# Optimization experiments

Hardware: AMD Instinct MI355X
Metric: run time of the kernel (lower is better)

Reference implementation:

```python
import jax, jax.numpy as jnp
import numpy as np

GLYPH_DIM = 4096
PADDING_IDX = GLYPH_DIM  # 4096
GLYPH_EMB = 20           # CHAR_EMB 16 + COLOR_EMB 4
HIDDEN = 32
MAX_LEN = 64


def setup_inputs() -> dict:
    key = jax.random.key(0)
    k1, k2, k3, k4, k5, k6, k7 = jax.random.split(key, 7)
    B, H, W = 8192, 21, 79
    glyph_chars = jax.random.randint(k1, (B, H, W), 0, 256, dtype=jnp.int32)
    glyph_colors = jax.random.randint(k2, (B, H, W), 0, 16, dtype=jnp.int32)
    # Embedding table with zero padding row (torch padding_idx semantics)
    emb_table = jax.random.normal(k3, (GLYPH_DIM + 1, GLYPH_EMB), dtype=jnp.float32) * 0.02
    emb_table = emb_table.at[PADDING_IDX].set(0.0)
    s = 1.0 / np.sqrt(HIDDEN)
    W_ih = jax.random.uniform(k4, (HIDDEN, GLYPH_EMB), minval=-s, maxval=s, dtype=jnp.float32)
    W_hh = jax.random.uniform(k5, (HIDDEN, HIDDEN), minval=-s, maxval=s, dtype=jnp.float32)
    b_ih = jax.random.uniform(k6, (HIDDEN,), minval=-s, maxval=s, dtype=jnp.float32)
    b_hh = jax.random.uniform(k7, (HIDDEN,), minval=-s, maxval=s, dtype=jnp.float32)
    return {"glyph_chars": glyph_chars, "glyph_colors": glyph_colors,
            "emb_table": emb_table, "W_ih": W_ih, "W_hh": W_hh,
            "b_ih": b_ih, "b_hh": b_hh}


def _encode_bag(glyph_chars, glyph_colors):
    """Batched sorted-unique compaction over the bounded glyph id range."""
    B = glyph_chars.shape[0]
    g_ids = ((glyph_chars << 4) + glyph_colors).reshape(B, -1)  # [B, H*W]
    # presence[b, g] = glyph g appears in sample b (batched histogram)
    bidx = jnp.broadcast_to(jnp.arange(B, dtype=g_ids.dtype)[:, None], g_ids.shape)
    presence = jnp.zeros((B, GLYPH_DIM), dtype=bool).at[bidx, g_ids].set(True)
    # compact: present ids keep their value, absent become PADDING_IDX (=4096),
    # so sorting yields ascending unique ids followed by padding.
    ids = jnp.arange(GLYPH_DIM, dtype=jnp.int32)
    keys = jnp.where(presence, ids, jnp.int32(PADDING_IDX))
    bag = jnp.sort(keys, axis=1)[:, :MAX_LEN]  # [B, MAX_LEN]
    lengths = jnp.minimum(presence.sum(axis=1), MAX_LEN)  # [B]
    return bag, lengths


def reference(glyph_chars, glyph_colors, emb_table, W_ih, W_hh, b_ih, b_hh):
    bag, lengths = _encode_bag(glyph_chars, glyph_colors)
    emb = emb_table[bag]  # [B, MAX_LEN, GLYPH_EMB]
    B = emb.shape[0]

    # packed RNN == plain RNN where hidden state freezes past each sequence length
    xs = jnp.swapaxes(emb, 0, 1)  # [T, B, E]

    def step(h, inp):
        xt, t = inp
        h_new = jnp.tanh(xt @ W_ih.T + b_ih + h @ W_hh.T + b_hh)
        h = jnp.where((t < lengths)[:, None], h_new, h)
        return h, None

    h0 = jnp.zeros((B, HIDDEN), dtype=emb.dtype)
    h, _ = jax.lax.scan(step, h0, (xs, jnp.arange(MAX_LEN)))
    return (h, emb, bag)
```

## Files before the change

### kernel.cpp

```cpp
#include <hip/hip_runtime.h>

#define HW 1659
#define PADID 4096
#define EMB 20
#define HID 32
#define MAXLEN 64

typedef float v2f __attribute__((ext_vector_type(2)));

template <int CTRL>
__device__ __forceinline__ float dppf(float v) {
    return __builtin_bit_cast(float,
        __builtin_amdgcn_update_dpp(0, __builtin_bit_cast(int, v),
                                    CTRL, 0xF, 0xF, true));
}
#define DPP_XOR1 0xB1
#define DPP_XOR2 0x4E
#define DPP_XOR7 0x141
#define DPP_XORF 0x140

__global__ __launch_bounds__(128) void proj_kernel(
    const float* __restrict__ emb_table, const float* __restrict__ W_ih,
    float* __restrict__ proj)
{
    const int tid = threadIdx.x;
    const int g = blockIdx.x * 4 + (tid >> 5);
    const int j = tid & 31;
    if (g > PADID) return;
    const float* er = emb_table + (size_t)g * EMB;
    const float* wr = W_ih + j * EMB;
    float s = 0.f;
#pragma unroll
    for (int k = 0; k < EMB; k++) s += wr[k] * er[k];
    proj[(size_t)g * HID + j] = s;
}

__global__ __launch_bounds__(256) void bag_emb_kernel(
    const int* __restrict__ chars, const int* __restrict__ colors,
    const float* __restrict__ emb_table,
    float* __restrict__ out_emb, float* __restrict__ out_bag)
{
    __shared__ unsigned char pres[4096];
    __shared__ int bagl[64];
    __shared__ int wsum[4];

    const int b   = blockIdx.x;
    const int tid = threadIdx.x;
    const int lane = tid & 63;
    const int wv   = tid >> 6;

    const int base = b * HW;
    const int pe = (4 - (base & 3)) & 3;
    const int nv = (HW - pe) >> 2;
    const int nt = HW - pe - (nv << 2);
    const int4* c4 = (const int4*)(chars + base + pe);
    const int4* k4 = (const int4*)(colors + base + pe);

    int4 ca = c4[tid], ka = k4[tid];
    const bool has2 = (tid + 256) < nv;
    const int i2 = has2 ? tid + 256 : tid;
    int4 cb = c4[i2], kb = k4[i2];
    int gp = -1, gt = -1;
    if (tid < pe) gp = (chars[base + tid] << 4) + colors[base + tid];
    if (tid < nt) {
        int i = base + pe + (nv << 2) + tid;
        gt = (chars[i] << 4) + colors[i];
    }

    ((uint4*)pres)[tid] = make_uint4(0u, 0u, 0u, 0u);
    if (tid < 64) bagl[tid] = PADID;
    __syncthreads();

    pres[(ca.x << 4) + ka.x] = 1;
    pres[(ca.y << 4) + ka.y] = 1;
    pres[(ca.z << 4) + ka.z] = 1;
    pres[(ca.w << 4) + ka.w] = 1;
    if (has2) {
        pres[(cb.x << 4) + kb.x] = 1;
        pres[(cb.y << 4) + kb.y] = 1;
        pres[(cb.z << 4) + kb.z] = 1;
        pres[(cb.w << 4) + kb.w] = 1;
    }
    if (gp >= 0) pres[gp] = 1;
    if (gt >= 0) pres[gt] = 1;
    __syncthreads();

    uint4 w4 = ((const uint4*)pres)[tid];
    const unsigned M = 0x01010101u;
    int cnt = __popc(w4.x & M) + __popc(w4.y & M)
            + __popc(w4.z & M) + __popc(w4.w & M);

    int pre = cnt;
#pragma unroll
    for (int d = 1; d < 64; d <<= 1) {
        int v = __shfl_up(pre, d, 64);
        if (lane >= d) pre += v;
    }
    if (lane == 63) wsum[wv] = pre;
    __syncthreads();
    int wbase = 0;
#pragma unroll
    for (int w2 = 0; w2 < 4; w2++) wbase += (w2 < wv) ? wsum[w2] : 0;
    int p = wbase + pre - cnt;

    unsigned wrd[4] = {w4.x, w4.y, w4.z, w4.w};
#pragma unroll
    for (int c = 0; c < 4; c++) {
#pragma unroll
        for (int k = 0; k < 4; k++) {
            if ((wrd[c] >> (8 * k)) & 1) {
                if (p < 64) bagl[p] = 16 * tid + 4 * c + k;
                p++;
            }
        }
    }
    __syncthreads();

    if (tid < 64) out_bag[(size_t)b * 64 + tid] = (float)bagl[tid];

    const float4* tab4 = (const float4*)emb_table;
    float4* dst4 = (float4*)(out_emb + (size_t)b * (MAXLEN * EMB));
    for (int q = tid; q < MAXLEN * 5; q += 256) {
        int t = q / 5;
        int m = q - t * 5;
        int row = bagl[t];
        dst4[q] = tab4[row * 5 + m];
    }
}

__global__ __launch_bounds__(128)
__attribute__((amdgpu_waves_per_eu(2, 2)))
void rnn_kernel(
    const float* __restrict__ proj, const float* __restrict__ bagf,
    const float* __restrict__ W_hh,
    const float* __restrict__ b_ih, const float* __restrict__ b_hh,
    float* __restrict__ out_h)
{
    const int tid  = threadIdx.x;
    const int wv   = tid >> 6;
    const int lane = tid & 63;
    const int sl   = lane >> 4;
    const int ib   = wv * 4 + sl;
    const int jj   = lane & 15;
    const int b    = blockIdx.x * 8 + ib;

    const int GMAP[16] = {0,1,2,3, 7,6,5,4, 15,14,13,12,11,10,9,8};

    v2f w0[16], w1[16];
    const float2* wr0 = (const float2*)(W_hh + (2 * jj) * HID);
    const float2* wr1 = (const float2*)(W_hh + (2 * jj + 1) * HID);
#pragma unroll
    for (int m = 0; m < 16; m++) {
        const int c = jj ^ GMAP[m];
        float2 a = wr0[c], bb = wr1[c];
        w0[m] = (v2f){a.x, a.y};
        w1[m] = (v2f){bb.x, bb.y};
    }
    const float sb0 = b_ih[2 * jj]     + b_hh[2 * jj];
    const float sb1 = b_ih[2 * jj + 1] + b_hh[2 * jj + 1];

    const float* bps = bagf + (size_t)b * 64;
    const float2* proj2 = (const float2*)proj;

    float h0 = 0.f, h1 = 0.f;

#pragma unroll
    for (int ch = 0; ch < 4; ch++) {
        int idx[16];
#pragma unroll
        for (int i = 0; i < 16; i++) idx[i] = (int)bps[ch * 16 + i];
        float2 pv[16];
#pragma unroll
        for (int i = 0; i < 16; i++) pv[i] = proj2[idx[i] * 16 + jj];

#pragma unroll
        for (int i = 0; i < 16; i++) {
            const bool upd = idx[i] < PADID;

            v2f g[16];
            g[0] = (v2f){h0, h1};
            g[1] = (v2f){dppf<DPP_XOR1>(g[0].x), dppf<DPP_XOR1>(g[0].y)};
            g[2] = (v2f){dppf<DPP_XOR2>(g[0].x), dppf<DPP_XOR2>(g[0].y)};
            g[3] = (v2f){dppf<DPP_XOR2>(g[1].x), dppf<DPP_XOR2>(g[1].y)};
#pragma unroll
            for (int m = 0; m < 4; m++)
                g[4 + m] = (v2f){dppf<DPP_XOR7>(g[m].x), dppf<DPP_XOR7>(g[m].y)};
#pragma unroll
            for (int m = 0; m < 8; m++)
                g[8 + m] = (v2f){dppf<DPP_XORF>(g[m].x), dppf<DPP_XORF>(g[m].y)};

            v2f a0 = (v2f){0.f, 0.f}, b0 = a0, a1 = a0, b1 = a0;
#pragma unroll
            for (int m = 0; m < 16; m += 2) {
                a0 = __builtin_elementwise_fma(w0[m],     g[m],     a0);
                b0 = __builtin_elementwise_fma(w0[m + 1], g[m + 1], b0);
                a1 = __builtin_elementwise_fma(w1[m],     g[m],     a1);
                b1 = __builtin_elementwise_fma(w1[m + 1], g[m + 1], b1);
            }
            float s0 = sb0 + pv[i].x + (a0.x + a0.y) + (b0.x + b0.y);
            float s1 = sb1 + pv[i].y + (a1.x + a1.y) + (b1.x + b1.y);

            float e0 = __expf(2.f * s0);
            float e1 = __expf(2.f * s1);
            float th0 = 1.f - 2.f * __builtin_amdgcn_rcpf(e0 + 1.f);
            float th1 = 1.f - 2.f * __builtin_amdgcn_rcpf(e1 + 1.f);

            h0 = upd ? th0 : h0;
            h1 = upd ? th1 : h1;
        }
    }

    ((float2*)(out_h + (size_t)b * HID))[jj] = make_float2(h0, h1);
}

__global__ __launch_bounds__(128, 4) void rnn_kernel_noproj(
    const float* __restrict__ emb, const float* __restrict__ bagf,
    const float* __restrict__ W_ih, const float* __restrict__ W_hh,
    const float* __restrict__ b_ih, const float* __restrict__ b_hh,
    float* __restrict__ out_h)
{
    __shared__ float hbuf[4][32];
    const int tid = threadIdx.x;
    const int ib  = tid >> 5;
    const int j   = tid & 31;
    const int b   = blockIdx.x * 4 + ib;

    float wih[EMB];
#pragma unroll
    for (int k = 0; k < EMB; k++) wih[k] = W_ih[j * EMB + k];
    float whh[HID];
#pragma unroll
    for (int k = 0; k < HID; k++) whh[k] = W_hh[j * HID + k];
    const float sbias = b_ih[j] + b_hh[j];

    const float* bp = bagf + (size_t)b * 64;
    unsigned long long m0 = __ballot(bp[j]      < 4095.5f);
    unsigned long long m1 = __ballot(bp[32 + j] < 4095.5f);
    const int half = ib & 1;
    const int len = __popc((unsigned)(m0 >> (half * 32)))
                  + __popc((unsigned)(m1 >> (half * 32)));

    hbuf[ib][j] = 0.f;
    asm volatile("s_waitcnt lgkmcnt(0)" ::: "memory");

    float h = 0.f;
    const float* xb = emb + (size_t)b * (MAXLEN * EMB);
    for (int t = 0; t < MAXLEN; t++) {
        const float4* xp = (const float4*)(xb + t * EMB);
        float4 x0 = xp[0], x1 = xp[1], x2 = xp[2], x3 = xp[3], x4 = xp[4];
        float s = sbias;
        const float4* hb4 = (const float4*)hbuf[ib];
#pragma unroll
        for (int m = 0; m < 8; m++) {
            float4 hv = hb4[m];
            s += whh[4*m+0]*hv.x + whh[4*m+1]*hv.y
               + whh[4*m+2]*hv.z + whh[4*m+3]*hv.w;
        }
        s += wih[0]*x0.x + wih[1]*x0.y + wih[2]*x0.z + wih[3]*x0.w;
        s += wih[4]*x1.x + wih[5]*x1.y + wih[6]*x1.z + wih[7]*x1.w;
        s += wih[8]*x2.x + wih[9]*x2.y + wih[10]*x2.z + wih[11]*x2.w;
        s += wih[12]*x3.x + wih[13]*x3.y + wih[14]*x3.z + wih[15]*x3.w;
        s += wih[16]*x4.x + wih[17]*x4.y + wih[18]*x4.z + wih[19]*x4.w;
        s = fminf(fmaxf(s, -9.f), 9.f);
        float e = __expf(2.f * s);
        float th = (e - 1.f) * __builtin_amdgcn_rcpf(e + 1.f);
        h = (t < len) ? th : h;
        hbuf[ib][j] = h;
        asm volatile("s_waitcnt lgkmcnt(0)" ::: "memory");
    }
    out_h[(size_t)b * HID + j] = h;
}

extern "C" void kernel_launch(void* const* d_in, const int* in_sizes, int n_in,
                              void* d_out, int out_size, void* d_ws, size_t ws_size,
                              hipStream_t stream) {
    const int*   chars     = (const int*)d_in[0];
    const int*   colors    = (const int*)d_in[1];
    const float* emb_table = (const float*)d_in[2];
    const float* W_ih      = (const float*)d_in[3];
    const float* W_hh      = (const float*)d_in[4];
    const float* b_ih      = (const float*)d_in[5];
    const float* b_hh      = (const float*)d_in[6];

    const int B = in_sizes[0] / HW;

    float* out     = (float*)d_out;
    float* out_h   = out;
    float* out_emb = out + (size_t)B * HID;
    float* out_bag = out_emb + (size_t)B * MAXLEN * EMB;

    const size_t proj_bytes = (size_t)(PADID + 1) * HID * sizeof(float);

    bag_emb_kernel<<<B, 256, 0, stream>>>(chars, colors, emb_table, out_emb, out_bag);

    if (ws_size >= proj_bytes) {
        float* proj = (float*)d_ws;
        proj_kernel<<<(PADID + 1 + 3) / 4, 128, 0, stream>>>(emb_table, W_ih, proj);
        rnn_kernel<<<B / 8, 128, 0, stream>>>(proj, out_bag, W_hh, b_ih, b_hh, out_h);
    } else {
        rnn_kernel_noproj<<<B / 4, 128, 0, stream>>>(out_emb, out_bag, W_ih, W_hh,
                                                     b_ih, b_hh, out_h);
    }
}
```

Measured before the change: 179.8 us.

## Assign one wave per bag sample and fuse projection into bag kernel

Restructures the bag/embedding kernel so each 64-lane wave handles one sample with its own 4KB presence table, which drops the block-wide __syncthreads and the cross-wave scan. The compaction now scans the presence table in four chunks and stops early once 64 ids are found. The separate proj_kernel launch is folded in as extra tail blocks of the same grid, saving one launch. In exchange each block uses 16KB of LDS, which can limit occupancy, and each wave issues more sequential loads per sample.

```diff
diff --git a/kernel.cpp b/kernel.cpp
--- a/kernel.cpp
+++ b/kernel.cpp
@@ -5,6 +5,7 @@
 #define EMB 20
 #define HID 32
 #define MAXLEN 64
+#define PROJ_BLOCKS 64
 
 typedef float v2f __attribute__((ext_vector_type(2)));
 
@@ -19,35 +20,40 @@
 #define DPP_XOR7 0x141
 #define DPP_XORF 0x140
 
-__global__ __launch_bounds__(128) void proj_kernel(
+__global__ __launch_bounds__(256, 8) void bag_emb_wave_kernel(
+    const int* __restrict__ chars, const int* __restrict__ colors,
     const float* __restrict__ emb_table, const float* __restrict__ W_ih,
-    float* __restrict__ proj)
+    float* __restrict__ out_emb, float* __restrict__ out_bag,
+    float* __restrict__ proj, int nbag, int Btot)
 {
-    const int tid = threadIdx.x;
-    const int g = blockIdx.x * 4 + (tid >> 5);
-    const int j = tid & 31;
-    if (g > PADID) return;
-    const float* er = emb_table + (size_t)g * EMB;
-    const float* wr = W_ih + j * EMB;
-    float s = 0.f;
-#pragma unroll
-    for (int k = 0; k < EMB; k++) s += wr[k] * er[k];
-    proj[(size_t)g * HID + j] = s;
-}
-
-__global__ __launch_bounds__(256) void bag_emb_kernel(
-    const int* __restrict__ chars, const int* __restrict__ colors,
-    const float* __restrict__ emb_table,
-    float* __restrict__ out_emb, float* __restrict__ out_bag)
-{
-    __shared__ unsigned char pres[4096];
-    __shared__ int bagl[64];
-    __shared__ int wsum[4];
-
-    const int b   = blockIdx.x;
-    const int tid = threadIdx.x;
+    if ((int)blockIdx.x >= nbag) {
+        const int gid = ((int)blockIdx.x - nbag) * 256 + threadIdx.x;
+        const int NP = (PADID + 1) * HID;
+        for (int idx = gid; idx < NP; idx += PROJ_BLOCKS * 256) {
+            const int g = idx >> 5, j = idx & 31;
+            const float* er = emb_table + (size_t)g * EMB;
+            const float* wr = W_ih + j * EMB;
+            float s = 0.f;
+#pragma unroll
+            for (int k = 0; k < EMB; k++) s += wr[k] * er[k];
+            proj[idx] = s;
+        }
+        return;
+    }
+
+    __shared__ __align__(16) unsigned char pres[4][4096];
+    __shared__ int bagl[4][64];
+
+    const int tid  = threadIdx.x;
+    const int wv   = tid >> 6;
     const int lane = tid & 63;
-    const int wv   = tid >> 6;
+    const int b    = (int)blockIdx.x * 4 + wv;
+    if (b >= Btot) return;
+
+    uint4* pz = (uint4*)pres[wv];
+#pragma unroll
+    for (int r = 0; r < 4; r++) pz[lane + (r << 6)] = make_uint4(0u, 0u, 0u, 0u);
+    bagl[wv][lane] = PADID;
 
     const int base = b * HW;
     const int pe = (4 - (base & 3)) & 3;
@@ -56,75 +62,75 @@
     const int4* c4 = (const int4*)(chars + base + pe);
     const int4* k4 = (const int4*)(colors + base + pe);
 
-    int4 ca = c4[tid], ka = k4[tid];
-    const bool has2 = (tid + 256) < nv;
-    const int i2 = has2 ? tid + 256 : tid;
-    int4 cb = c4[i2], kb = k4[i2];
     int gp = -1, gt = -1;
-    if (tid < pe) gp = (chars[base + tid] << 4) + colors[base + tid];
-    if (tid < nt) {
-        int i = base + pe + (nv << 2) + tid;
+    if (lane < pe) gp = (chars[base + lane] << 4) + colors[base + lane];
+    if (lane < nt) {
+        const int i = base + pe + (nv << 2) + lane;
         gt = (chars[i] << 4) + colors[i];
     }
 
-    ((uint4*)pres)[tid] = make_uint4(0u, 0u, 0u, 0u);
-    if (tid < 64) bagl[tid] = PADID;
-    __syncthreads();
-
-    pres[(ca.x << 4) + ka.x] = 1;
-    pres[(ca.y << 4) + ka.y] = 1;
-    pres[(ca.z << 4) + ka.z] = 1;
-    pres[(ca.w << 4) + ka.w] = 1;
-    if (has2) {
-        pres[(cb.x << 4) + kb.x] = 1;
-        pres[(cb.y << 4) + kb.y] = 1;
-        pres[(cb.z << 4) + kb.z] = 1;
-        pres[(cb.w << 4) + kb.w] = 1;
-    }
-    if (gp >= 0) pres[gp] = 1;
-    if (gt >= 0) pres[gt] = 1;
-    __syncthreads();
-
-    uint4 w4 = ((const uint4*)pres)[tid];
+    unsigned char* pw = pres[wv];
+#pragma unroll
+    for (int k = 0; k < 7; k++) {
+        const int i = lane + (k << 6);
+        if (i < nv) {
+            const int4 c = c4[i], kk = k4[i];
+            pw[(c.x << 4) + kk.x] = 1;
+            pw[(c.y << 4) + kk.y] = 1;
+            pw[(c.z << 4) + kk.z] = 1;
+            pw[(c.w << 4) + kk.w] = 1;
+        }
+    }
+    if (gp >= 0) pw[gp] = 1;
+    if (gt >= 0) pw[gt] = 1;
+
+    asm volatile("s_waitcnt lgkmcnt(0)" ::: "memory");
+
     const unsigned M = 0x01010101u;
-    int cnt = __popc(w4.x & M) + __popc(w4.y & M)
-            + __popc(w4.z & M) + __popc(w4.w & M);
-
-    int pre = cnt;
-#pragma unroll
-    for (int d = 1; d < 64; d <<= 1) {
-        int v = __shfl_up(pre, d, 64);
-        if (lane >= d) pre += v;
-    }
-    if (lane == 63) wsum[wv] = pre;
-    __syncthreads();
-    int wbase = 0;
-#pragma unroll
-    for (int w2 = 0; w2 < 4; w2++) wbase += (w2 < wv) ? wsum[w2] : 0;
-    int p = wbase + pre - cnt;
-
-    unsigned wrd[4] = {w4.x, w4.y, w4.z, w4.w};
-#pragma unroll
-    for (int c = 0; c < 4; c++) {
-#pragma unroll
-        for (int k = 0; k < 4; k++) {
-            if ((wrd[c] >> (8 * k)) & 1) {
-                if (p < 64) bagl[p] = 16 * tid + 4 * c + k;
-                p++;
+    int base_cnt = 0;
+#pragma unroll 1
+    for (int r = 0; r < 4; r++) {
+        const uint4 w = ((const uint4*)pres[wv])[lane + (r << 6)];
+        const int cnt = __popc(w.x & M) + __popc(w.y & M)
+                      + __popc(w.z & M) + __popc(w.w & M);
+        int pre = cnt;
+#pragma unroll
+        for (int d = 1; d < 64; d <<= 1) {
+            const int v = __shfl_up(pre, d, 64);
+            if (lane >= d) pre += v;
+        }
+        int p = base_cnt + pre - cnt;
+        if (p < 64 && cnt) {
+            const unsigned wd[4] = {w.x, w.y, w.z, w.w};
+            const int idbase = (r << 10) + (lane << 4);
+#pragma unroll
+            for (int c = 0; c < 4; c++) {
+                unsigned m = wd[c] & M;
+                while (m) {
+                    const int bit = __ffs((int)m) - 1;
+                    if (p < 64) bagl[wv][p] = idbase + (c << 2) + (bit >> 3);
+                    p++;
+                    m &= m - 1;
+                }
             }
         }
-    }
-    __syncthreads();
-
-    if (tid < 64) out_bag[(size_t)b * 64 + tid] = (float)bagl[tid];
+        base_cnt += __shfl(pre, 63, 64);
+        if (base_cnt >= 64) break;
+    }
+
+    asm volatile("s_waitcnt lgkmcnt(0)" ::: "memory");
+
+    out_bag[(size_t)b * 64 + lane] = (float)bagl[wv][lane];
 
     const float4* tab4 = (const float4*)emb_table;
     float4* dst4 = (float4*)(out_emb + (size_t)b * (MAXLEN * EMB));
-    for (int q = tid; q < MAXLEN * 5; q += 256) {
-        int t = q / 5;
-        int m = q - t * 5;
-        int row = bagl[t];
-        dst4[q] = tab4[row * 5 + m];
+#pragma unroll
+    for (int m5 = 0; m5 < 5; m5++) {
+        const int q = lane + (m5 << 6);
+        const int t = q / 5;
+        const int mm = q - t * 5;
+        const int row = bagl[wv][t];
+        dst4[q] = tab4[row * 5 + mm];
     }
 }
 
@@ -283,6 +289,7 @@
     const float* b_hh      = (const float*)d_in[6];
 
     const int B = in_sizes[0] / HW;
+    const int NBAG = (B + 3) / 4;
 
     float* out     = (float*)d_out;
     float* out_h   = out;
@@ -291,13 +298,14 @@
 
     const size_t proj_bytes = (size_t)(PADID + 1) * HID * sizeof(float);
 
-    bag_emb_kernel<<<B, 256, 0, stream>>>(chars, colors, emb_table, out_emb, out_bag);
-
-    if (ws_size >= proj_bytes) {
+    if (ws_size >= proj_bytes && (B % 8) == 0) {
         float* proj = (float*)d_ws;
-        proj_kernel<<<(PADID + 1 + 3) / 4, 128, 0, stream>>>(emb_table, W_ih, proj);
+        bag_emb_wave_kernel<<<NBAG + PROJ_BLOCKS, 256, 0, stream>>>(
+            chars, colors, emb_table, W_ih, out_emb, out_bag, proj, NBAG, B);
         rnn_kernel<<<B / 8, 128, 0, stream>>>(proj, out_bag, W_hh, b_ih, b_hh, out_h);
     } else {
+        bag_emb_wave_kernel<<<NBAG, 256, 0, stream>>>(
+            chars, colors, emb_table, W_ih, out_emb, out_bag, (float*)d_ws, NBAG, B);
         rnn_kernel_noproj<<<B / 4, 128, 0, stream>>>(out_emb, out_bag, W_ih, W_hh,
                                                      b_ih, b_hh, out_h);
     }
```

Result: slower. 204.3 us (+13.7%).

## Fuse projection into bag kernel, halve block size, early-exit scan

Applied to the files above, without the earlier changes.

Merges the proj_kernel launch into bag_emb_kernel by appending extra blocks that compute the embedding-times-W_ih table, which removes one kernel launch. The bag kernel drops from 256 to 128 threads per block, so each thread loads four int4 vectors instead of two. The presence scan now walks the 4096-entry bitmap in two halves and stops once 64 unique ids have been found. The aim is lower launch overhead and less scan work, at the cost of more per-thread work and an extra barrier per half of the scan.

```diff
diff --git a/kernel.cpp b/kernel.cpp
--- a/kernel.cpp
+++ b/kernel.cpp
@@ -5,6 +5,7 @@
 #define EMB 20
 #define HID 32
 #define MAXLEN 64
+#define PROJ_BLOCKS 128
 
 typedef float v2f __attribute__((ext_vector_type(2)));
 
@@ -19,35 +20,36 @@
 #define DPP_XOR7 0x141
 #define DPP_XORF 0x140
 
-__global__ __launch_bounds__(128) void proj_kernel(
+__global__ __launch_bounds__(128, 4) void bag_emb_kernel(
+    const int* __restrict__ chars, const int* __restrict__ colors,
     const float* __restrict__ emb_table, const float* __restrict__ W_ih,
-    float* __restrict__ proj)
+    float* __restrict__ out_emb, float* __restrict__ out_bag,
+    float* __restrict__ proj, int nbag)
 {
     const int tid = threadIdx.x;
-    const int g = blockIdx.x * 4 + (tid >> 5);
-    const int j = tid & 31;
-    if (g > PADID) return;
-    const float* er = emb_table + (size_t)g * EMB;
-    const float* wr = W_ih + j * EMB;
-    float s = 0.f;
-#pragma unroll
-    for (int k = 0; k < EMB; k++) s += wr[k] * er[k];
-    proj[(size_t)g * HID + j] = s;
-}
-
-__global__ __launch_bounds__(256) void bag_emb_kernel(
-    const int* __restrict__ chars, const int* __restrict__ colors,
-    const float* __restrict__ emb_table,
-    float* __restrict__ out_emb, float* __restrict__ out_bag)
-{
-    __shared__ unsigned char pres[4096];
+
+    if ((int)blockIdx.x >= nbag) {
+        const int gid = ((int)blockIdx.x - nbag) * 128 + tid;
+        const int NP = (PADID + 1) * HID;
+        for (int idx = gid; idx < NP; idx += PROJ_BLOCKS * 128) {
+            const int g = idx >> 5, j = idx & 31;
+            const float* er = emb_table + (size_t)g * EMB;
+            const float* wr = W_ih + j * EMB;
+            float s = 0.f;
+#pragma unroll
+            for (int k = 0; k < EMB; k++) s += wr[k] * er[k];
+            proj[idx] = s;
+        }
+        return;
+    }
+
+    __shared__ __align__(16) unsigned char pres[4096];
     __shared__ int bagl[64];
-    __shared__ int wsum[4];
-
-    const int b   = blockIdx.x;
-    const int tid = threadIdx.x;
+    __shared__ int wsum[2];
+
     const int lane = tid & 63;
     const int wv   = tid >> 6;
+    const int b    = blockIdx.x;
 
     const int base = b * HW;
     const int pe = (4 - (base & 3)) & 3;
@@ -56,63 +58,80 @@
     const int4* c4 = (const int4*)(chars + base + pe);
     const int4* k4 = (const int4*)(colors + base + pe);
 
-    int4 ca = c4[tid], ka = k4[tid];
-    const bool has2 = (tid + 256) < nv;
-    const int i2 = has2 ? tid + 256 : tid;
-    int4 cb = c4[i2], kb = k4[i2];
+    int4 ca0 = c4[tid],       ka0 = k4[tid];
+    int4 ca1 = c4[tid + 128], ka1 = k4[tid + 128];
+    int4 ca2 = c4[tid + 256], ka2 = k4[tid + 256];
+    const bool has3 = (tid + 384) < nv;
+    const int i3 = has3 ? tid + 384 : tid;
+    int4 ca3 = c4[i3], ka3 = k4[i3];
     int gp = -1, gt = -1;
     if (tid < pe) gp = (chars[base + tid] << 4) + colors[base + tid];
     if (tid < nt) {
-        int i = base + pe + (nv << 2) + tid;
+        const int i = base + pe + (nv << 2) + tid;
         gt = (chars[i] << 4) + colors[i];
     }
 
-    ((uint4*)pres)[tid] = make_uint4(0u, 0u, 0u, 0u);
+    ((uint4*)pres)[tid]       = make_uint4(0u, 0u, 0u, 0u);
+    ((uint4*)pres)[tid + 128] = make_uint4(0u, 0u, 0u, 0u);
     if (tid < 64) bagl[tid] = PADID;
     __syncthreads();
 
-    pres[(ca.x << 4) + ka.x] = 1;
-    pres[(ca.y << 4) + ka.y] = 1;
-    pres[(ca.z << 4) + ka.z] = 1;
-    pres[(ca.w << 4) + ka.w] = 1;
-    if (has2) {
-        pres[(cb.x << 4) + kb.x] = 1;
-        pres[(cb.y << 4) + kb.y] = 1;
-        pres[(cb.z << 4) + kb.z] = 1;
-        pres[(cb.w << 4) + kb.w] = 1;
+    pres[(ca0.x << 4) + ka0.x] = 1;
+    pres[(ca0.y << 4) + ka0.y] = 1;
+    pres[(ca0.z << 4) + ka0.z] = 1;
+    pres[(ca0.w << 4) + ka0.w] = 1;
+    pres[(ca1.x << 4) + ka1.x] = 1;
+    pres[(ca1.y << 4) + ka1.y] = 1;
+    pres[(ca1.z << 4) + ka1.z] = 1;
+    pres[(ca1.w << 4) + ka1.w] = 1;
+    pres[(ca2.x << 4) + ka2.x] = 1;
+    pres[(ca2.y << 4) + ka2.y] = 1;
+    pres[(ca2.z << 4) + ka2.z] = 1;
+    pres[(ca2.w << 4) + ka2.w] = 1;
+    if (has3) {
+        pres[(ca3.x << 4) + ka3.x] = 1;
+        pres[(ca3.y << 4) + ka3.y] = 1;
+        pres[(ca3.z << 4) + ka3.z] = 1;
+        pres[(ca3.w << 4) + ka3.w] = 1;
     }
     if (gp >= 0) pres[gp] = 1;
     if (gt >= 0) pres[gt] = 1;
     __syncthreads();
 
-    uint4 w4 = ((const uint4*)pres)[tid];
     const unsigned M = 0x01010101u;
-    int cnt = __popc(w4.x & M) + __popc(w4.y & M)
-            + __popc(w4.z & M) + __popc(w4.w & M);
-
-    int pre = cnt;
-#pragma unroll
-    for (int d = 1; d < 64; d <<= 1) {
-        int v = __shfl_up(pre, d, 64);
-        if (lane >= d) pre += v;
-    }
-    if (lane == 63) wsum[wv] = pre;
-    __syncthreads();
-    int wbase = 0;
-#pragma unroll
-    for (int w2 = 0; w2 < 4; w2++) wbase += (w2 < wv) ? wsum[w2] : 0;
-    int p = wbase + pre - cnt;
-
-    unsigned wrd[4] = {w4.x, w4.y, w4.z, w4.w};
-#pragma unroll
-    for (int c = 0; c < 4; c++) {
-#pragma unroll
-        for (int k = 0; k < 4; k++) {
-            if ((wrd[c] >> (8 * k)) & 1) {
-                if (p < 64) bagl[p] = 16 * tid + 4 * c + k;
-                p++;
+    int base_cnt = 0;
+#pragma unroll 1
+    for (int r = 0; r < 2; r++) {
+        const uint4 w = ((const uint4*)pres)[tid + (r << 7)];
+        const int cnt = __popc(w.x & M) + __popc(w.y & M)
+                      + __popc(w.z & M) + __popc(w.w & M);
+        int pre = cnt;
+#pragma unroll
+        for (int d = 1; d < 64; d <<= 1) {
+            const int v = __shfl_up(pre, d, 64);
+            if (lane >= d) pre += v;
+        }
+        if (lane == 63) wsum[wv] = pre;
+        __syncthreads();
+        const int w0 = wsum[0], w1 = wsum[1];
+        int p = base_cnt + (wv ? w0 : 0) + pre - cnt;
+        if (p < 64) {
+            const unsigned wrd[4] = {w.x, w.y, w.z, w.w};
+            const int idbase = (r << 11) + (tid << 4);
+#pragma unroll
+            for (int c = 0; c < 4; c++) {
+#pragma unroll
+                for (int k = 0; k < 4; k++) {
+                    if ((wrd[c] >> (8 * k)) & 1) {
+                        if (p < 64) bagl[p] = idbase + 4 * c + k;
+                        p++;
+                    }
+                }
             }
         }
+        base_cnt += w0 + w1;
+        if (base_cnt >= 64) break;
+        __syncthreads();
     }
     __syncthreads();
 
@@ -120,11 +139,15 @@
 
     const float4* tab4 = (const float4*)emb_table;
     float4* dst4 = (float4*)(out_emb + (size_t)b * (MAXLEN * EMB));
-    for (int q = tid; q < MAXLEN * 5; q += 256) {
-        int t = q / 5;
-        int m = q - t * 5;
-        int row = bagl[t];
-        dst4[q] = tab4[row * 5 + m];
+#pragma unroll
+    for (int m = 0; m < 3; m++) {
+        const int q = tid + (m << 7);
+        if (q < MAXLEN * 5) {
+            const int t = q / 5;
+            const int mm = q - t * 5;
+            const int row = bagl[t];
+            dst4[q] = tab4[row * 5 + mm];
+        }
     }
 }
 
@@ -291,13 +314,14 @@
 
     const size_t proj_bytes = (size_t)(PADID + 1) * HID * sizeof(float);
 
-    bag_emb_kernel<<<B, 256, 0, stream>>>(chars, colors, emb_table, out_emb, out_bag);
-
-    if (ws_size >= proj_bytes) {
+    if (ws_size >= proj_bytes && (B % 8) == 0) {
         float* proj = (float*)d_ws;
-        proj_kernel<<<(PADID + 1 + 3) / 4, 128, 0, stream>>>(emb_table, W_ih, proj);
+        bag_emb_kernel<<<B + PROJ_BLOCKS, 128, 0, stream>>>(
+            chars, colors, emb_table, W_ih, out_emb, out_bag, proj, B);
         rnn_kernel<<<B / 8, 128, 0, stream>>>(proj, out_bag, W_hh, b_ih, b_hh, out_h);
     } else {
+        bag_emb_kernel<<<B, 128, 0, stream>>>(
+            chars, colors, emb_table, W_ih, out_emb, out_bag, (float*)d_ws, B);
         rnn_kernel_noproj<<<B / 4, 128, 0, stream>>>(out_emb, out_bag, W_ih, W_hh,
                                                      b_ih, b_hh, out_h);
     }
```

New measurement: 180.2 us. No clear change (+0.2%).
